# Performance work log

Hardware: AMD Instinct MI355X
Metric: run time of the kernel (lower is better)

Reference implementation:

```python
import jax, jax.numpy as jnp
import numpy as np

N_HEADS = 16

def setup_inputs() -> dict:
    key = jax.random.key(0)
    qkv = jax.random.normal(key, (8, 3072, 1024), dtype=jnp.float32)
    return {"qkv": qkv}

def reference(qkv) -> jnp.ndarray:
    B, D, L = qkv.shape
    q, k, v = jnp.split(qkv, 3, axis=1)            # each [B, H*ch, L]
    ch = D // (3 * N_HEADS)
    scale = 1.0 / np.sqrt(np.sqrt(ch)).astype(np.float32)
    q = (q * scale).reshape(B * N_HEADS, ch, L)
    k = (k * scale).reshape(B * N_HEADS, ch, L)
    v = v.reshape(B * N_HEADS, ch, L)
    weight = jnp.einsum('bct,bcs->bts', q, k)       # [B*H, L, L]
    weight = jax.nn.softmax(weight, axis=-1)
    z = jnp.einsum('bts,bcs->bct', weight, v)       # [B*H, ch, L]
    return z.reshape(B, -1, L)
```

## Files before the change

kernel.cpp:

```cpp
#include <hip/hip_runtime.h>


typedef __attribute__((ext_vector_type(8))) _Float16 f16x8;
typedef __attribute__((ext_vector_type(4))) _Float16 f16x4;
typedef __attribute__((ext_vector_type(4))) float f32x4;

#define MAT_HALVES 8388608
#define WS_BYTES   50331648

#define ASYNC16(g, l) __builtin_amdgcn_global_load_lds(                    \
    (__attribute__((address_space(1))) void*)(void*)(g),                   \
    (__attribute__((address_space(3))) void*)(void*)(l), 16, 0, 0)

__global__ __launch_bounds__(256) void prepass_kernel(
    const float* __restrict__ qkv, _Float16* __restrict__ ws) {
    __shared__ float ft[64][68];
    const int tid = threadIdx.x;
    const int bid = blockIdx.x;
    const int mat = bid >> 11;
    const int idx = bid & 2047;
    const int head = idx >> 4;
    const int blk  = idx & 15;
    const int b = head >> 4, h = head & 15;
    const float* src = qkv + (size_t)b * 3072 * 1024
                           + (size_t)(mat * 1024 + h * 64) * 1024;
    if (mat < 2) {
        const int t0 = blk * 64;
        const float scale = (mat == 0) ? (0.125f * 1.44269504f) : 1.0f;
#pragma unroll
        for (int i = 0; i < 4; ++i) {
            const int c = i * 16 + (tid >> 4);
            const int t = (tid & 15) * 4;
            const float4 v = *(const float4*)(src + (size_t)c * 1024 + t0 + t);
            ft[t + 0][c] = v.x * scale;
            ft[t + 1][c] = v.y * scale;
            ft[t + 2][c] = v.z * scale;
            ft[t + 3][c] = v.w * scale;
        }
        __syncthreads();
        _Float16* dst = ws + (size_t)mat * MAT_HALVES
                           + (size_t)head * 65536 + (size_t)t0 * 64;
#pragma unroll
        for (int r = 0; r < 2; ++r) {
            const int g = r * 256 + tid;
            const int t = g >> 3, cb = g & 7;
            const float4 a = *(const float4*)&ft[t][cb * 8];
            const float4 bq = *(const float4*)&ft[t][cb * 8 + 4];
            f16x8 o = { (_Float16)a.x,  (_Float16)a.y,  (_Float16)a.z,  (_Float16)a.w,
                        (_Float16)bq.x, (_Float16)bq.y, (_Float16)bq.z, (_Float16)bq.w };
            *(f16x8*)(dst + (size_t)t * 64 + (size_t)(cb ^ (t & 7)) * 8) = o;
        }
    } else {
        const int s0 = blk * 64;
        _Float16* dst = ws + (size_t)2 * MAT_HALVES + (size_t)head * 65536;
#pragma unroll
        for (int i = 0; i < 4; ++i) {
            const int c = i * 16 + (tid >> 4);
            const int s = (tid & 15) * 4;
            const float4 v = *(const float4*)(src + (size_t)c * 1024 + s0 + s);
            f16x4 o = { (_Float16)v.x, (_Float16)v.y, (_Float16)v.z, (_Float16)v.w };
            const int sb = s >> 3, pos = s & 7;
            *(f16x4*)(dst + (size_t)c * 1024 + s0 + (size_t)((sb ^ (c & 7)) * 8 + pos)) = o;
        }
    }
}

__launch_bounds__(256, 2)
__global__ void attn_kernel(const _Float16* __restrict__ ws,
                            float* __restrict__ out) {
    __shared__ __align__(16) _Float16 KV[2][8192];
    __shared__ __align__(16) _Float16 P[256][72];

    const int tid  = threadIdx.x;
    const int wv   = tid >> 6;
    const int lane = tid & 63;
    const int li   = lane & 15;
    const int quad = lane >> 4;

    const int bid  = blockIdx.x;
    const int head = (bid >> 5) * 8 + (bid & 7);
    const int tt   = (bid >> 3) & 3;
    const int t0   = tt * 256;

    const _Float16* qh = ws + (size_t)head * 65536 + (size_t)t0 * 64;
    const _Float16* kt = ws + MAT_HALVES + (size_t)head * 65536;
    const _Float16* vh = ws + 2 * (size_t)MAT_HALVES + (size_t)head * 65536;

    _Float16* Ql = &KV[0][0];
#pragma unroll
    for (int j = 0; j < 8; ++j) {
        const int g0 = (wv * 8 + j) * 512;
        ASYNC16(qh + g0 + lane * 8, Ql + g0);
    }
    __syncthreads();

    f16x8 bqf[4][2];
#pragma unroll
    for (int sub = 0; sub < 4; ++sub) {
        const int row = wv * 64 + sub * 16 + li;
#pragma unroll
        for (int kk = 0; kk < 2; ++kk) {
            const int cb = (kk * 4 + quad) ^ (li & 7);
            bqf[sub][kk] = *(const f16x8*)&Ql[row * 64 + cb * 8];
        }
    }
    __syncthreads();

    f32x4 accz[4][4] = {};
    float psum[4] = {};

#pragma unroll
    for (int j = 0; j < 2; ++j) {
        const int g0 = (wv * 2 + j) * 64;
        ASYNC16(kt + (size_t)(g0 + lane) * 8, &KV[0][g0 * 8]);
        const int g = g0 + lane;
        ASYNC16(vh + (size_t)(g >> 3) * 1024 + (size_t)(g & 7) * 8,
                &KV[0][4096 + g0 * 8]);
    }

    for (int si = 0; si < 16; ++si) {
        __syncthreads();
        if (si < 15) {
            const int s0n = (si + 1) * 64;
            const int nb = (si + 1) & 1;
#pragma unroll
            for (int j = 0; j < 2; ++j) {
                const int g0 = (wv * 2 + j) * 64;
                ASYNC16(kt + (size_t)s0n * 64 + (size_t)(g0 + lane) * 8,
                        &KV[nb][g0 * 8]);
                const int g = g0 + lane;
                ASYNC16(vh + (size_t)(g >> 3) * 1024 + s0n + (size_t)(g & 7) * 8,
                        &KV[nb][4096 + g0 * 8]);
            }
        }
        const _Float16* Kl = &KV[si & 1][0];
        const _Float16* Vl = &KV[si & 1][4096];

#pragma unroll
        for (int ns = 0; ns < 4; ++ns) {
            f16x8 ak[2];
#pragma unroll
            for (int kk = 0; kk < 2; ++kk) {
                const int cb = (kk * 4 + quad) ^ (li & 7);
                ak[kk] = *(const f16x8*)&Kl[(ns * 16 + li) * 64 + cb * 8];
            }
#pragma unroll
            for (int sub = 0; sub < 4; ++sub) {
                f32x4 st = {};
                st = __builtin_amdgcn_mfma_f32_16x16x32_f16(ak[0], bqf[sub][0], st, 0, 0, 0);
                st = __builtin_amdgcn_mfma_f32_16x16x32_f16(ak[1], bqf[sub][1], st, 0, 0, 0);
                const float p0 = __builtin_amdgcn_exp2f(st[0]);
                const float p1 = __builtin_amdgcn_exp2f(st[1]);
                const float p2 = __builtin_amdgcn_exp2f(st[2]);
                const float p3 = __builtin_amdgcn_exp2f(st[3]);
                psum[sub] += (p0 + p1) + (p2 + p3);
                f16x4 pk = { (_Float16)p0, (_Float16)p1, (_Float16)p2, (_Float16)p3 };
                *(f16x4*)&P[wv * 64 + sub * 16 + li][ns * 16 + quad * 4] = pk;
            }
        }

#pragma unroll
        for (int kk = 0; kk < 2; ++kk) {
            f16x8 ap[4];
#pragma unroll
            for (int sub = 0; sub < 4; ++sub)
                ap[sub] = *(const f16x8*)&P[wv * 64 + sub * 16 + li][kk * 32 + quad * 8];
#pragma unroll
            for (int nc = 0; nc < 4; ++nc) {
                const int cb = (kk * 4 + quad) ^ (li & 7);
                f16x8 bv = *(const f16x8*)&Vl[(nc * 16 + li) * 64 + cb * 8];
#pragma unroll
                for (int sub = 0; sub < 4; ++sub)
                    accz[sub][nc] = __builtin_amdgcn_mfma_f32_16x16x32_f16(
                        ap[sub], bv, accz[sub][nc], 0, 0, 0);
            }
        }
    }

    float rl[4][4];
#pragma unroll
    for (int sub = 0; sub < 4; ++sub) {
        float s = psum[sub];
        s += __shfl_xor(s, 16);
        s += __shfl_xor(s, 32);
#pragma unroll
        for (int r = 0; r < 4; ++r)
            rl[sub][r] = 1.0f / __shfl(s, quad * 4 + r);
    }

    float* obase = out + (size_t)(head >> 4) * 1024 * 1024
                       + (size_t)((head & 15) * 64) * 1024 + t0;
#pragma unroll
    for (int sub = 0; sub < 4; ++sub)
#pragma unroll
        for (int nc = 0; nc < 4; ++nc) {
            const int c = nc * 16 + li;
            const int t = wv * 64 + sub * 16 + quad * 4;
            f32x4 z = accz[sub][nc];
            float4 o = { z[0] * rl[sub][0], z[1] * rl[sub][1],
                         z[2] * rl[sub][2], z[3] * rl[sub][3] };
            *(float4*)(obase + (size_t)c * 1024 + t) = o;
        }
}

struct S1fb {
    _Float16 K[64][72];
    _Float16 V[64][72];
    _Float16 P[128][72];
};
union SMemFb {
    S1fb s1;
    float zt[64][132];
};

__launch_bounds__(256, 4)
__global__ void qkv_attn_fallback(const float* __restrict__ qkv,
                                  float* __restrict__ out) {
    constexpr int L = 1024;
    __shared__ SMemFb sm;
    const int tid  = threadIdx.x;
    const int wv   = tid >> 6;
    const int lane = tid & 63;
    const int li   = lane & 15;
    const int quad = lane >> 4;
    const int bid  = blockIdx.x;
    const int head = (bid >> 6) * 8 + (bid & 7);
    const int tt   = (bid >> 3) & 7;
    const int b = head >> 4;
    const int h = head & 15;
    const float* qbase = qkv + (size_t)b * 3072 * L + (size_t)(h * 64) * L;
    const float* kbase = qbase + (size_t)1024 * L;
    const float* vbase = qbase + (size_t)2048 * L;
    float*       obase = out + (size_t)b * 1024 * L + (size_t)(h * 64) * L;
    const int t0 = tt * 128;
#pragma unroll
    for (int i = 0; i < 4; ++i) {
        const int c = i * 16 + (tid >> 4);
        const int t = (tid & 15) * 8;
        const float4 qa = *(const float4*)(qbase + (size_t)c * L + t0 + t);
        const float4 qb = *(const float4*)(qbase + (size_t)c * L + t0 + t + 4);
        sm.s1.P[t + 0][c] = (_Float16)(qa.x * 0.125f);
        sm.s1.P[t + 1][c] = (_Float16)(qa.y * 0.125f);
        sm.s1.P[t + 2][c] = (_Float16)(qa.z * 0.125f);
        sm.s1.P[t + 3][c] = (_Float16)(qa.w * 0.125f);
        sm.s1.P[t + 4][c] = (_Float16)(qb.x * 0.125f);
        sm.s1.P[t + 5][c] = (_Float16)(qb.y * 0.125f);
        sm.s1.P[t + 6][c] = (_Float16)(qb.z * 0.125f);
        sm.s1.P[t + 7][c] = (_Float16)(qb.w * 0.125f);
    }
    __syncthreads();
    f16x8 aq0[2], aq1[2];
#pragma unroll
    for (int kk = 0; kk < 2; ++kk) {
        aq0[kk] = *(const f16x8*)&sm.s1.P[wv * 32 + li][kk * 32 + quad * 8];
        aq1[kk] = *(const f16x8*)&sm.s1.P[wv * 32 + 16 + li][kk * 32 + quad * 8];
    }
    f32x4 accz0[4] = {}, accz1[4] = {};
    float psum0[4] = {}, psum1[4] = {};
    float4 kreg[4], vreg[4];
#pragma unroll
    for (int i = 0; i < 4; ++i) {
        const int c = i * 16 + (tid >> 4);
        const int s = (tid & 15) * 4;
        kreg[i] = *(const float4*)(kbase + (size_t)c * L + s);
        vreg[i] = *(const float4*)(vbase + (size_t)c * L + s);
    }
    for (int si = 0; si < 16; ++si) {
        __syncthreads();
#pragma unroll
        for (int i = 0; i < 4; ++i) {
            const int c = i * 16 + (tid >> 4);
            const int s = (tid & 15) * 4;
            sm.s1.K[s + 0][c] = (_Float16)kreg[i].x;
            sm.s1.K[s + 1][c] = (_Float16)kreg[i].y;
            sm.s1.K[s + 2][c] = (_Float16)kreg[i].z;
            sm.s1.K[s + 3][c] = (_Float16)kreg[i].w;
            f16x4 pv = { (_Float16)vreg[i].x, (_Float16)vreg[i].y,
                         (_Float16)vreg[i].z, (_Float16)vreg[i].w };
            *(f16x4*)&sm.s1.V[c][s] = pv;
        }
        __syncthreads();
        if (si < 15) {
            const int s0n = (si + 1) * 64;
#pragma unroll
            for (int i = 0; i < 4; ++i) {
                const int c = i * 16 + (tid >> 4);
                const int s = (tid & 15) * 4;
                kreg[i] = *(const float4*)(kbase + (size_t)c * L + s0n + s);
                vreg[i] = *(const float4*)(vbase + (size_t)c * L + s0n + s);
            }
        }
#pragma unroll
        for (int nt = 0; nt < 4; ++nt) {
            f32x4 a0 = {}, a1 = {};
#pragma unroll
            for (int kk = 0; kk < 2; ++kk) {
                f16x8 bk = *(const f16x8*)&sm.s1.K[nt * 16 + li][kk * 32 + quad * 8];
                a0 = __builtin_amdgcn_mfma_f32_16x16x32_f16(aq0[kk], bk, a0, 0, 0, 0);
                a1 = __builtin_amdgcn_mfma_f32_16x16x32_f16(aq1[kk], bk, a1, 0, 0, 0);
            }
#pragma unroll
            for (int r = 0; r < 4; ++r) {
                const float p0 = __expf(a0[r]);
                const float p1 = __expf(a1[r]);
                psum0[r] += p0;
                psum1[r] += p1;
                sm.s1.P[wv * 32 + quad * 4 + r][nt * 16 + li] = (_Float16)p0;
                sm.s1.P[wv * 32 + 16 + quad * 4 + r][nt * 16 + li] = (_Float16)p1;
            }
        }
#pragma unroll
        for (int kk = 0; kk < 2; ++kk) {
            f16x8 ap0 = *(const f16x8*)&sm.s1.P[wv * 32 + li][kk * 32 + quad * 8];
            f16x8 ap1 = *(const f16x8*)&sm.s1.P[wv * 32 + 16 + li][kk * 32 + quad * 8];
#pragma unroll
            for (int nt = 0; nt < 4; ++nt) {
                f16x8 bv = *(const f16x8*)&sm.s1.V[nt * 16 + li][kk * 32 + quad * 8];
                accz0[nt] = __builtin_amdgcn_mfma_f32_16x16x32_f16(ap0, bv, accz0[nt], 0, 0, 0);
                accz1[nt] = __builtin_amdgcn_mfma_f32_16x16x32_f16(ap1, bv, accz1[nt], 0, 0, 0);
            }
        }
    }
    float rl0[4], rl1[4];
#pragma unroll
    for (int r = 0; r < 4; ++r) {
        float s0 = psum0[r], s1 = psum1[r];
        s0 += __shfl_xor(s0, 1); s0 += __shfl_xor(s0, 2);
        s0 += __shfl_xor(s0, 4); s0 += __shfl_xor(s0, 8);
        s1 += __shfl_xor(s1, 1); s1 += __shfl_xor(s1, 2);
        s1 += __shfl_xor(s1, 4); s1 += __shfl_xor(s1, 8);
        rl0[r] = 1.0f / s0;
        rl1[r] = 1.0f / s1;
    }
    __syncthreads();
#pragma unroll
    for (int nt = 0; nt < 4; ++nt)
#pragma unroll
        for (int r = 0; r < 4; ++r) {
            sm.zt[nt * 16 + li][wv * 32 + quad * 4 + r]      = accz0[nt][r] * rl0[r];
            sm.zt[nt * 16 + li][wv * 32 + 16 + quad * 4 + r] = accz1[nt][r] * rl1[r];
        }
    __syncthreads();
#pragma unroll
    for (int i = 0; i < 8; ++i) {
        const int c = i * 8 + (tid >> 5);
        const int t = (tid & 31) * 4;
        float4 o = { sm.zt[c][t], sm.zt[c][t + 1],
                     sm.zt[c][t + 2], sm.zt[c][t + 3] };
        *(float4*)(obase + (size_t)c * L + t0 + t) = o;
    }
}

extern "C" void kernel_launch(void* const* d_in, const int* in_sizes, int n_in,
                              void* d_out, int out_size, void* d_ws, size_t ws_size,
                              hipStream_t stream) {
    const float* qkv = (const float*)d_in[0];
    float* out = (float*)d_out;
    if (ws_size >= (size_t)WS_BYTES) {
        _Float16* ws = (_Float16*)d_ws;
        prepass_kernel<<<6144, 256, 0, stream>>>(qkv, ws);
        attn_kernel<<<512, 256, 0, stream>>>(ws, out);
    } else {
        qkv_attn_fallback<<<1024, 256, 0, stream>>>(qkv, out);
    }
}
```

Measured before the change: 201.8 us.

## Fuse Q and V fp16 conversion into attention kernel, prepass only K

The prepass now converts only K to transposed fp16. The attention kernel reads Q directly from fp32 input, transposes and scales it through shared memory into registers, and streams V from fp32 global memory via registers, converting to fp16 into the LDS double buffer each iteration. This removes the workspace write and re-read of Q and V and shrinks the prepass grid. In exchange V loads become synchronous register loads that must be hidden behind the MFMA work, and the kernel gains register pressure and extra barriers.

Result: no change. 201.4 us (-0.2%).

```diff
diff --git a/kernel.cpp b/kernel.cpp
--- a/kernel.cpp
+++ b/kernel.cpp
@@ -5,68 +5,50 @@
 typedef __attribute__((ext_vector_type(4))) _Float16 f16x4;
 typedef __attribute__((ext_vector_type(4))) float f32x4;
 
-#define MAT_HALVES 8388608
-#define WS_BYTES   50331648
+#define WS_BYTES 16777216
 
 #define ASYNC16(g, l) __builtin_amdgcn_global_load_lds(                    \
     (__attribute__((address_space(1))) void*)(void*)(g),                   \
     (__attribute__((address_space(3))) void*)(void*)(l), 16, 0, 0)
 
-__global__ __launch_bounds__(256) void prepass_kernel(
+__global__ __launch_bounds__(256) void prepass_k(
     const float* __restrict__ qkv, _Float16* __restrict__ ws) {
     __shared__ float ft[64][68];
     const int tid = threadIdx.x;
     const int bid = blockIdx.x;
-    const int mat = bid >> 11;
-    const int idx = bid & 2047;
-    const int head = idx >> 4;
-    const int blk  = idx & 15;
+    const int head = bid >> 4;
+    const int blk  = bid & 15;
     const int b = head >> 4, h = head & 15;
     const float* src = qkv + (size_t)b * 3072 * 1024
-                           + (size_t)(mat * 1024 + h * 64) * 1024;
-    if (mat < 2) {
-        const int t0 = blk * 64;
-        const float scale = (mat == 0) ? (0.125f * 1.44269504f) : 1.0f;
-#pragma unroll
-        for (int i = 0; i < 4; ++i) {
-            const int c = i * 16 + (tid >> 4);
-            const int t = (tid & 15) * 4;
-            const float4 v = *(const float4*)(src + (size_t)c * 1024 + t0 + t);
-            ft[t + 0][c] = v.x * scale;
-            ft[t + 1][c] = v.y * scale;
-            ft[t + 2][c] = v.z * scale;
-            ft[t + 3][c] = v.w * scale;
-        }
-        __syncthreads();
-        _Float16* dst = ws + (size_t)mat * MAT_HALVES
-                           + (size_t)head * 65536 + (size_t)t0 * 64;
-#pragma unroll
-        for (int r = 0; r < 2; ++r) {
-            const int g = r * 256 + tid;
-            const int t = g >> 3, cb = g & 7;
-            const float4 a = *(const float4*)&ft[t][cb * 8];
-            const float4 bq = *(const float4*)&ft[t][cb * 8 + 4];
-            f16x8 o = { (_Float16)a.x,  (_Float16)a.y,  (_Float16)a.z,  (_Float16)a.w,
-                        (_Float16)bq.x, (_Float16)bq.y, (_Float16)bq.z, (_Float16)bq.w };
-            *(f16x8*)(dst + (size_t)t * 64 + (size_t)(cb ^ (t & 7)) * 8) = o;
-        }
-    } else {
-        const int s0 = blk * 64;
-        _Float16* dst = ws + (size_t)2 * MAT_HALVES + (size_t)head * 65536;
-#pragma unroll
-        for (int i = 0; i < 4; ++i) {
-            const int c = i * 16 + (tid >> 4);
-            const int s = (tid & 15) * 4;
-            const float4 v = *(const float4*)(src + (size_t)c * 1024 + s0 + s);
-            f16x4 o = { (_Float16)v.x, (_Float16)v.y, (_Float16)v.z, (_Float16)v.w };
-            const int sb = s >> 3, pos = s & 7;
-            *(f16x4*)(dst + (size_t)c * 1024 + s0 + (size_t)((sb ^ (c & 7)) * 8 + pos)) = o;
-        }
+                           + (size_t)(1024 + h * 64) * 1024;
+    const int s0 = blk * 64;
+#pragma unroll
+    for (int i = 0; i < 4; ++i) {
+        const int c = i * 16 + (tid >> 4);
+        const int s = (tid & 15) * 4;
+        const float4 v = *(const float4*)(src + (size_t)c * 1024 + s0 + s);
+        ft[s + 0][c] = v.x;
+        ft[s + 1][c] = v.y;
+        ft[s + 2][c] = v.z;
+        ft[s + 3][c] = v.w;
+    }
+    __syncthreads();
+    _Float16* dst = ws + (size_t)head * 65536 + (size_t)s0 * 64;
+#pragma unroll
+    for (int r = 0; r < 2; ++r) {
+        const int g = r * 256 + tid;
+        const int t = g >> 3, cb = g & 7;
+        const float4 a = *(const float4*)&ft[t][cb * 8];
+        const float4 bq = *(const float4*)&ft[t][cb * 8 + 4];
+        f16x8 o = { (_Float16)a.x,  (_Float16)a.y,  (_Float16)a.z,  (_Float16)a.w,
+                    (_Float16)bq.x, (_Float16)bq.y, (_Float16)bq.z, (_Float16)bq.w };
+        *(f16x8*)(dst + (size_t)t * 64 + (size_t)(cb ^ (t & 7)) * 8) = o;
     }
 }
 
 __launch_bounds__(256, 2)
-__global__ void attn_kernel(const _Float16* __restrict__ ws,
+__global__ void attn_kernel(const float* __restrict__ qkv,
+                            const _Float16* __restrict__ ws,
                             float* __restrict__ out) {
     __shared__ __align__(16) _Float16 KV[2][8192];
     __shared__ __align__(16) _Float16 P[256][72];
@@ -82,55 +64,87 @@
     const int tt   = (bid >> 3) & 3;
     const int t0   = tt * 256;
 
-    const _Float16* qh = ws + (size_t)head * 65536 + (size_t)t0 * 64;
-    const _Float16* kt = ws + MAT_HALVES + (size_t)head * 65536;
-    const _Float16* vh = ws + 2 * (size_t)MAT_HALVES + (size_t)head * 65536;
-
-    _Float16* Ql = &KV[0][0];
-#pragma unroll
-    for (int j = 0; j < 8; ++j) {
-        const int g0 = (wv * 8 + j) * 512;
-        ASYNC16(qh + g0 + lane * 8, Ql + g0);
-    }
-    __syncthreads();
-
-    f16x8 bqf[4][2];
-#pragma unroll
-    for (int sub = 0; sub < 4; ++sub) {
-        const int row = wv * 64 + sub * 16 + li;
-#pragma unroll
-        for (int kk = 0; kk < 2; ++kk) {
-            const int cb = (kk * 4 + quad) ^ (li & 7);
-            bqf[sub][kk] = *(const f16x8*)&Ql[row * 64 + cb * 8];
-        }
-    }
-    __syncthreads();
-
-    f32x4 accz[4][4] = {};
-    float psum[4] = {};
+    const int b = head >> 4, h = head & 15;
+    const float* qsrc = qkv + (size_t)b * 3072 * 1024 + (size_t)(h * 64) * 1024;
+    const float* vsrc = qkv + (size_t)b * 3072 * 1024 + (size_t)(2048 + h * 64) * 1024;
+    const _Float16* kt = ws + (size_t)head * 65536;
+
+    const int sc = (tid >> 4);
+    const int s4 = (tid & 15) * 4;
 
 #pragma unroll
     for (int j = 0; j < 2; ++j) {
         const int g0 = (wv * 2 + j) * 64;
         ASYNC16(kt + (size_t)(g0 + lane) * 8, &KV[0][g0 * 8]);
-        const int g = g0 + lane;
-        ASYNC16(vh + (size_t)(g >> 3) * 1024 + (size_t)(g & 7) * 8,
-                &KV[0][4096 + g0 * 8]);
-    }
+    }
+    float4 vreg[4];
+#pragma unroll
+    for (int i = 0; i < 4; ++i) {
+        const int c = i * 16 + sc;
+        vreg[i] = *(const float4*)(vsrc + (size_t)c * 1024 + s4);
+    }
+
+    float (*ft)[68] = (float (*)[68])&P[0][0];
+    const float qscale = 0.125f * 1.44269504f;
+    f16x8 bqf[4][2];
+#pragma unroll
+    for (int ct = 0; ct < 4; ++ct) {
+#pragma unroll
+        for (int i = 0; i < 4; ++i) {
+            const int c = i * 16 + sc;
+            const int t = (tid & 15) * 4;
+            const float4 v = *(const float4*)(qsrc + (size_t)c * 1024 + t0 + ct * 64 + t);
+            ft[t + 0][c] = v.x * qscale;
+            ft[t + 1][c] = v.y * qscale;
+            ft[t + 2][c] = v.z * qscale;
+            ft[t + 3][c] = v.w * qscale;
+        }
+        __syncthreads();
+        if (wv == ct) {
+#pragma unroll
+            for (int sub = 0; sub < 4; ++sub) {
+                const int tl = sub * 16 + li;
+#pragma unroll
+                for (int kk = 0; kk < 2; ++kk) {
+                    const int c0 = (kk * 4 + quad) * 8;
+                    const float4 a = *(const float4*)&ft[tl][c0];
+                    const float4 b2 = *(const float4*)&ft[tl][c0 + 4];
+                    bqf[sub][kk] = f16x8{ (_Float16)a.x,  (_Float16)a.y,
+                                          (_Float16)a.z,  (_Float16)a.w,
+                                          (_Float16)b2.x, (_Float16)b2.y,
+                                          (_Float16)b2.z, (_Float16)b2.w };
+                }
+            }
+        }
+        __syncthreads();
+    }
+
+#pragma unroll
+    for (int i = 0; i < 4; ++i) {
+        const int c = i * 16 + sc;
+        f16x4 pv = { (_Float16)vreg[i].x, (_Float16)vreg[i].y,
+                     (_Float16)vreg[i].z, (_Float16)vreg[i].w };
+        *(f16x4*)&KV[0][4096 + c * 64 + (((s4 >> 3) ^ (c & 7)) << 3) + (s4 & 7)] = pv;
+    }
+
+    f32x4 accz[4][4] = {};
+    float psum[4] = {};
 
     for (int si = 0; si < 16; ++si) {
         __syncthreads();
+        const int nb = (si + 1) & 1;
         if (si < 15) {
             const int s0n = (si + 1) * 64;
-            const int nb = (si + 1) & 1;
 #pragma unroll
             for (int j = 0; j < 2; ++j) {
                 const int g0 = (wv * 2 + j) * 64;
                 ASYNC16(kt + (size_t)s0n * 64 + (size_t)(g0 + lane) * 8,
                         &KV[nb][g0 * 8]);
-                const int g = g0 + lane;
-                ASYNC16(vh + (size_t)(g >> 3) * 1024 + s0n + (size_t)(g & 7) * 8,
-                        &KV[nb][4096 + g0 * 8]);
+            }
+#pragma unroll
+            for (int i = 0; i < 4; ++i) {
+                const int c = i * 16 + sc;
+                vreg[i] = *(const float4*)(vsrc + (size_t)c * 1024 + s0n + s4);
             }
         }
         const _Float16* Kl = &KV[si & 1][0];
@@ -175,6 +189,16 @@
                         ap[sub], bv, accz[sub][nc], 0, 0, 0);
             }
         }
+
+        if (si < 15) {
+#pragma unroll
+            for (int i = 0; i < 4; ++i) {
+                const int c = i * 16 + sc;
+                f16x4 pv = { (_Float16)vreg[i].x, (_Float16)vreg[i].y,
+                             (_Float16)vreg[i].z, (_Float16)vreg[i].w };
+                *(f16x4*)&KV[nb][4096 + c * 64 + (((s4 >> 3) ^ (c & 7)) << 3) + (s4 & 7)] = pv;
+            }
+        }
     }
 
     float rl[4][4];
@@ -188,8 +212,8 @@
             rl[sub][r] = 1.0f / __shfl(s, quad * 4 + r);
     }
 
-    float* obase = out + (size_t)(head >> 4) * 1024 * 1024
-                       + (size_t)((head & 15) * 64) * 1024 + t0;
+    float* obase = out + (size_t)b * 1024 * 1024
+                       + (size_t)(h * 64) * 1024 + t0;
 #pragma unroll
     for (int sub = 0; sub < 4; ++sub)
 #pragma unroll
@@ -358,8 +382,8 @@
     float* out = (float*)d_out;
     if (ws_size >= (size_t)WS_BYTES) {
         _Float16* ws = (_Float16*)d_ws;
-        prepass_kernel<<<6144, 256, 0, stream>>>(qkv, ws);
-        attn_kernel<<<512, 256, 0, stream>>>(ws, out);
+        prepass_k<<<2048, 256, 0, stream>>>(qkv, ws);
+        attn_kernel<<<512, 256, 0, stream>>>(qkv, ws, out);
     } else {
         qkv_attn_fallback<<<1024, 256, 0, stream>>>(qkv, out);
     }
```

## Fuse Q conversion into attention kernel and keep P in registers

Applied to the files above, without the earlier changes.

The prepass now converts only K and V to fp16. Q is loaded, scaled and converted inside the attention kernel through a shared-memory transpose. The attention block grows to 512 threads (8 waves of 32 query rows each), and the P tile stays in registers, feeding 16x16x16 MFMAs directly instead of round-tripping through LDS. This is meant to cut the workspace write and read traffic for Q and the LDS traffic for P, at the cost of more MFMA instructions (half the K depth) and a serial Q-staging phase with extra barriers.

Result: faster. 195.9 us (-3.0%).

```diff
diff --git a/kernel.cpp b/kernel.cpp
--- a/kernel.cpp
+++ b/kernel.cpp
@@ -6,13 +6,13 @@
 typedef __attribute__((ext_vector_type(4))) float f32x4;
 
 #define MAT_HALVES 8388608
-#define WS_BYTES   50331648
+#define WS_BYTES   33554432
 
 #define ASYNC16(g, l) __builtin_amdgcn_global_load_lds(                    \
     (__attribute__((address_space(1))) void*)(void*)(g),                   \
     (__attribute__((address_space(3))) void*)(void*)(l), 16, 0, 0)
 
-__global__ __launch_bounds__(256) void prepass_kernel(
+__global__ __launch_bounds__(256) void prepass_kv(
     const float* __restrict__ qkv, _Float16* __restrict__ ws) {
     __shared__ float ft[64][68];
     const int tid = threadIdx.x;
@@ -23,23 +23,21 @@
     const int blk  = idx & 15;
     const int b = head >> 4, h = head & 15;
     const float* src = qkv + (size_t)b * 3072 * 1024
-                           + (size_t)(mat * 1024 + h * 64) * 1024;
-    if (mat < 2) {
-        const int t0 = blk * 64;
-        const float scale = (mat == 0) ? (0.125f * 1.44269504f) : 1.0f;
+                           + (size_t)((1 + mat) * 1024 + h * 64) * 1024;
+    const int s0 = blk * 64;
+    if (mat == 0) {
 #pragma unroll
         for (int i = 0; i < 4; ++i) {
             const int c = i * 16 + (tid >> 4);
-            const int t = (tid & 15) * 4;
-            const float4 v = *(const float4*)(src + (size_t)c * 1024 + t0 + t);
-            ft[t + 0][c] = v.x * scale;
-            ft[t + 1][c] = v.y * scale;
-            ft[t + 2][c] = v.z * scale;
-            ft[t + 3][c] = v.w * scale;
+            const int s = (tid & 15) * 4;
+            const float4 v = *(const float4*)(src + (size_t)c * 1024 + s0 + s);
+            ft[s + 0][c] = v.x;
+            ft[s + 1][c] = v.y;
+            ft[s + 2][c] = v.z;
+            ft[s + 3][c] = v.w;
         }
         __syncthreads();
-        _Float16* dst = ws + (size_t)mat * MAT_HALVES
-                           + (size_t)head * 65536 + (size_t)t0 * 64;
+        _Float16* dst = ws + (size_t)head * 65536 + (size_t)s0 * 64;
 #pragma unroll
         for (int r = 0; r < 2; ++r) {
             const int g = r * 256 + tid;
@@ -51,8 +49,7 @@
             *(f16x8*)(dst + (size_t)t * 64 + (size_t)(cb ^ (t & 7)) * 8) = o;
         }
     } else {
-        const int s0 = blk * 64;
-        _Float16* dst = ws + (size_t)2 * MAT_HALVES + (size_t)head * 65536;
+        _Float16* dst = ws + (size_t)MAT_HALVES + (size_t)head * 65536;
 #pragma unroll
         for (int i = 0; i < 4; ++i) {
             const int c = i * 16 + (tid >> 4);
@@ -65,11 +62,14 @@
     }
 }
 
-__launch_bounds__(256, 2)
-__global__ void attn_kernel(const _Float16* __restrict__ ws,
+__launch_bounds__(512, 4)
+__global__ void attn_kernel(const float* __restrict__ qkv,
+                            const _Float16* __restrict__ ws,
                             float* __restrict__ out) {
-    __shared__ __align__(16) _Float16 KV[2][8192];
-    __shared__ __align__(16) _Float16 P[256][72];
+    __shared__ __align__(16) union SM {
+        _Float16 kv[2][8192];
+        float ft[64][68];
+    } sm;
 
     const int tid  = threadIdx.x;
     const int wv   = tid >> 6;
@@ -82,59 +82,65 @@
     const int tt   = (bid >> 3) & 3;
     const int t0   = tt * 256;
 
-    const _Float16* qh = ws + (size_t)head * 65536 + (size_t)t0 * 64;
-    const _Float16* kt = ws + MAT_HALVES + (size_t)head * 65536;
-    const _Float16* vh = ws + 2 * (size_t)MAT_HALVES + (size_t)head * 65536;
-
-    _Float16* Ql = &KV[0][0];
-#pragma unroll
-    for (int j = 0; j < 8; ++j) {
-        const int g0 = (wv * 8 + j) * 512;
-        ASYNC16(qh + g0 + lane * 8, Ql + g0);
-    }
-    __syncthreads();
-
-    f16x8 bqf[4][2];
-#pragma unroll
-    for (int sub = 0; sub < 4; ++sub) {
-        const int row = wv * 64 + sub * 16 + li;
-#pragma unroll
-        for (int kk = 0; kk < 2; ++kk) {
-            const int cb = (kk * 4 + quad) ^ (li & 7);
-            bqf[sub][kk] = *(const f16x8*)&Ql[row * 64 + cb * 8];
-        }
-    }
-    __syncthreads();
-
-    f32x4 accz[4][4] = {};
-    float psum[4] = {};
-
-#pragma unroll
-    for (int j = 0; j < 2; ++j) {
-        const int g0 = (wv * 2 + j) * 64;
-        ASYNC16(kt + (size_t)(g0 + lane) * 8, &KV[0][g0 * 8]);
-        const int g = g0 + lane;
-        ASYNC16(vh + (size_t)(g >> 3) * 1024 + (size_t)(g & 7) * 8,
-                &KV[0][4096 + g0 * 8]);
-    }
+    const int b = head >> 4, h = head & 15;
+    const float* qsrc = qkv + (size_t)b * 3072 * 1024 + (size_t)(h * 64) * 1024;
+    const _Float16* kt = ws + (size_t)head * 65536;
+    const _Float16* vh = ws + (size_t)MAT_HALVES + (size_t)head * 65536;
+
+    const float qscale = 0.125f * 1.44269504f;
+    f16x8 bqf[2][2];
+    {
+        const int ci = tid >> 4;
+        const int tq = (tid & 15) * 4;
+        for (int ct = 0; ct < 4; ++ct) {
+#pragma unroll
+            for (int i = 0; i < 2; ++i) {
+                const int c = i * 32 + ci;
+                const float4 v = *(const float4*)(qsrc + (size_t)c * 1024 + t0 + ct * 64 + tq);
+                sm.ft[tq + 0][c] = v.x * qscale;
+                sm.ft[tq + 1][c] = v.y * qscale;
+                sm.ft[tq + 2][c] = v.z * qscale;
+                sm.ft[tq + 3][c] = v.w * qscale;
+            }
+            __syncthreads();
+            if ((wv >> 1) == ct) {
+#pragma unroll
+                for (int sub = 0; sub < 2; ++sub) {
+                    const int tl = (wv & 1) * 32 + sub * 16 + li;
+#pragma unroll
+                    for (int kk = 0; kk < 2; ++kk) {
+                        const int c0 = (kk * 4 + quad) * 8;
+                        const float4 a  = *(const float4*)&sm.ft[tl][c0];
+                        const float4 b2 = *(const float4*)&sm.ft[tl][c0 + 4];
+                        bqf[sub][kk] = f16x8{ (_Float16)a.x,  (_Float16)a.y,
+                                              (_Float16)a.z,  (_Float16)a.w,
+                                              (_Float16)b2.x, (_Float16)b2.y,
+                                              (_Float16)b2.z, (_Float16)b2.w };
+                    }
+                }
+            }
+            __syncthreads();
+        }
+    }
+
+    ASYNC16(kt + (size_t)tid * 8, &sm.kv[0][tid * 8]);
+    ASYNC16(vh + (size_t)(tid >> 3) * 1024 + (size_t)(tid & 7) * 8,
+            &sm.kv[0][4096 + tid * 8]);
+
+    f32x4 accz[2][4] = {};
+    float psum[2] = {};
 
     for (int si = 0; si < 16; ++si) {
         __syncthreads();
         if (si < 15) {
             const int s0n = (si + 1) * 64;
             const int nb = (si + 1) & 1;
-#pragma unroll
-            for (int j = 0; j < 2; ++j) {
-                const int g0 = (wv * 2 + j) * 64;
-                ASYNC16(kt + (size_t)s0n * 64 + (size_t)(g0 + lane) * 8,
-                        &KV[nb][g0 * 8]);
-                const int g = g0 + lane;
-                ASYNC16(vh + (size_t)(g >> 3) * 1024 + s0n + (size_t)(g & 7) * 8,
-                        &KV[nb][4096 + g0 * 8]);
-            }
-        }
-        const _Float16* Kl = &KV[si & 1][0];
-        const _Float16* Vl = &KV[si & 1][4096];
+            ASYNC16(kt + (size_t)s0n * 64 + (size_t)tid * 8, &sm.kv[nb][tid * 8]);
+            ASYNC16(vh + (size_t)(tid >> 3) * 1024 + s0n + (size_t)(tid & 7) * 8,
+                    &sm.kv[nb][4096 + tid * 8]);
+        }
+        const _Float16* Kl = &sm.kv[si & 1][0];
+        const _Float16* Vl = &sm.kv[si & 1][4096];
 
 #pragma unroll
         for (int ns = 0; ns < 4; ++ns) {
@@ -144,8 +150,9 @@
                 const int cb = (kk * 4 + quad) ^ (li & 7);
                 ak[kk] = *(const f16x8*)&Kl[(ns * 16 + li) * 64 + cb * 8];
             }
-#pragma unroll
-            for (int sub = 0; sub < 4; ++sub) {
+            f16x4 pk[2];
+#pragma unroll
+            for (int sub = 0; sub < 2; ++sub) {
                 f32x4 st = {};
                 st = __builtin_amdgcn_mfma_f32_16x16x32_f16(ak[0], bqf[sub][0], st, 0, 0, 0);
                 st = __builtin_amdgcn_mfma_f32_16x16x32_f16(ak[1], bqf[sub][1], st, 0, 0, 0);
@@ -154,32 +161,26 @@
                 const float p2 = __builtin_amdgcn_exp2f(st[2]);
                 const float p3 = __builtin_amdgcn_exp2f(st[3]);
                 psum[sub] += (p0 + p1) + (p2 + p3);
-                f16x4 pk = { (_Float16)p0, (_Float16)p1, (_Float16)p2, (_Float16)p3 };
-                *(f16x4*)&P[wv * 64 + sub * 16 + li][ns * 16 + quad * 4] = pk;
-            }
-        }
-
-#pragma unroll
-        for (int kk = 0; kk < 2; ++kk) {
-            f16x8 ap[4];
-#pragma unroll
-            for (int sub = 0; sub < 4; ++sub)
-                ap[sub] = *(const f16x8*)&P[wv * 64 + sub * 16 + li][kk * 32 + quad * 8];
+                pk[sub] = f16x4{ (_Float16)p0, (_Float16)p1,
+                                 (_Float16)p2, (_Float16)p3 };
+            }
+            const int sb  = 2 * ns + (quad >> 1);
+            const int pos = (quad & 1) * 4;
 #pragma unroll
             for (int nc = 0; nc < 4; ++nc) {
-                const int cb = (kk * 4 + quad) ^ (li & 7);
-                f16x8 bv = *(const f16x8*)&Vl[(nc * 16 + li) * 64 + cb * 8];
-#pragma unroll
-                for (int sub = 0; sub < 4; ++sub)
-                    accz[sub][nc] = __builtin_amdgcn_mfma_f32_16x16x32_f16(
-                        ap[sub], bv, accz[sub][nc], 0, 0, 0);
-            }
-        }
-    }
-
-    float rl[4][4];
-#pragma unroll
-    for (int sub = 0; sub < 4; ++sub) {
+                const int c = nc * 16 + li;
+                f16x4 bv = *(const f16x4*)&Vl[c * 64 + ((sb ^ (c & 7)) << 3) + pos];
+                accz[0][nc] = __builtin_amdgcn_mfma_f32_16x16x16f16(
+                    pk[0], bv, accz[0][nc], 0, 0, 0);
+                accz[1][nc] = __builtin_amdgcn_mfma_f32_16x16x16f16(
+                    pk[1], bv, accz[1][nc], 0, 0, 0);
+            }
+        }
+    }
+
+    float rl[2][4];
+#pragma unroll
+    for (int sub = 0; sub < 2; ++sub) {
         float s = psum[sub];
         s += __shfl_xor(s, 16);
         s += __shfl_xor(s, 32);
@@ -188,14 +189,14 @@
             rl[sub][r] = 1.0f / __shfl(s, quad * 4 + r);
     }
 
-    float* obase = out + (size_t)(head >> 4) * 1024 * 1024
-                       + (size_t)((head & 15) * 64) * 1024 + t0;
-#pragma unroll
-    for (int sub = 0; sub < 4; ++sub)
+    float* obase = out + (size_t)b * 1024 * 1024
+                       + (size_t)(h * 64) * 1024 + t0;
+#pragma unroll
+    for (int sub = 0; sub < 2; ++sub)
 #pragma unroll
         for (int nc = 0; nc < 4; ++nc) {
             const int c = nc * 16 + li;
-            const int t = wv * 64 + sub * 16 + quad * 4;
+            const int t = wv * 32 + sub * 16 + quad * 4;
             f32x4 z = accz[sub][nc];
             float4 o = { z[0] * rl[sub][0], z[1] * rl[sub][1],
                          z[2] * rl[sub][2], z[3] * rl[sub][3] };
@@ -358,8 +359,8 @@
     float* out = (float*)d_out;
     if (ws_size >= (size_t)WS_BYTES) {
         _Float16* ws = (_Float16*)d_ws;
-        prepass_kernel<<<6144, 256, 0, stream>>>(qkv, ws);
-        attn_kernel<<<512, 256, 0, stream>>>(ws, out);
+        prepass_kv<<<4096, 256, 0, stream>>>(qkv, ws);
+        attn_kernel<<<512, 512, 0, stream>>>(qkv, ws, out);
     } else {
         qkv_attn_fallback<<<1024, 256, 0, stream>>>(qkv, out);
     }
```
